# Performance work log

Measured on AMD Instinct MI355X. Metric: run time of the kernel, lower is better.

The kernel has to match this reference:

```python
import jax, jax.numpy as jnp
import numpy as np

BS, NC, C, D, K, ALPHA = 4, 64, 256, 64, 32, 8
H_S, H_M, H_MOD = 256, 256, 256


def setup_inputs() -> dict:
    key = jax.random.key(0)
    ks = jax.random.split(key, 16)
    f = jax.random.normal
    return {
        "h": f(ks[0], (BS, NC, C, D)) * 0.1,
        "prev_messages": f(ks[1], (BS, NC, C, D)) * 0.1,
        "decay_logit": f(ks[2], (BS, NC, C)) * 0.1,
        "primitives_state": f(ks[3], (BS, NC, C, D)) * 0.1,
        "hebbian_traces": f(ks[4], (BS, NC, C, K)) * 0.1,
        "msg_magnitude": f(ks[5], (BS, NC, C)) * 0.1,
        "cc_signals": f(ks[6], (BS, NC * D)),
        "state_w1": f(ks[7], (H_S, 3 * D + 1)) * (2.0 / (3 * D + 1 + H_S)) ** 0.5,
        "state_b1": jnp.zeros((H_S,)),
        "state_w2": f(ks[8], (D, H_S)) * (2.0 / (H_S + D)) ** 0.5,
        "state_b2": jnp.zeros((D,)),
        "msg_w1": f(ks[9], (H_M, 3 * D)) * (2.0 / (3 * D + H_M)) ** 0.5,
        "msg_b1": jnp.zeros((H_M,)),
        "msg_w2": f(ks[10], (D, H_M)) * (2.0 / (H_M + D)) ** 0.5,
        "msg_b2": jnp.zeros((D,)),
        "mod_w1": f(ks[11], (NC, H_MOD, K + 3 * D + 1)) * (2.0 / (K + 3 * D + 1 + H_MOD)) ** 0.5,
        "mod_b1": jnp.zeros((NC, H_MOD)),
        "mod_w2": f(ks[12], (NC, H_MOD, K + 1 + D)) * (2.0 / (H_MOD + K + 1 + D)) ** 0.5,
        "mod_b2": jnp.zeros((NC, K + 1 + D)),
        "neuron_id": f(ks[13], (NC, C, D)) * (1.0 / D ** 0.5),
        "conn_indices": jax.random.randint(ks[14], (NC, C, K), 0, C, dtype=jnp.int32),
    }


def _forward(conn_indices, h, prev_messages, decay_logit, primitives_state,
             hebbian_traces, msg_magnitude, cc_signals,
             state_w1, state_b1, state_w2, state_b2,
             msg_w1, msg_b1, msg_w2, msg_b2,
             mod_w1, mod_b1, mod_w2, mod_b2, neuron_id):
    B = h.shape[0]
    # --- per-cell modulator: aggregate over neurons (dim 2), grouped GEMM over NC cells ---
    h_mean = h.mean(2)                                  # [B,NC,D]
    prim_mean = primitives_state.mean(2)                # [B,NC,D]
    hebb_mean = hebbian_traces.mean(2)                  # [B,NC,K]
    dec_mean = decay_logit.mean(2, keepdims=True)       # [B,NC,1]
    act = jnp.broadcast_to(msg_magnitude.mean(2)[..., None], (B, NC, D))
    mod_in = jnp.concatenate([hebb_mean, h_mean, dec_mean, prim_mean, act], -1)  # [B,NC,K+3D+1]
    hid = jnp.tanh(jnp.einsum('bci,chi->bch', mod_in, mod_w1) + mod_b1)
    out = jnp.einsum('bch,cho->bco', hid, mod_w2) + mod_b2                        # [B,NC,K+1+D]
    w_conn = out[..., :K]          # [B,NC,K] broadcast to all C neurons of the cell
    decay = out[..., K]            # [B,NC]
    prim = out[..., K + 1:]        # [B,NC,D]
    # --- cell-local K-neighbor weighted gather (memory bound) ---
    neigh = prev_messages[:, jnp.arange(NC)[:, None, None], conn_indices]   # [B,NC,C,K,D]
    w_sig = jax.nn.sigmoid(jnp.broadcast_to(w_conn[:, :, None, :], (B, NC, C, K)))
    received = jnp.einsum('bnck,bnckd->bncd', w_sig, neigh)                 # [B,NC,C,D]
    # --- inject external signal into the first ALPHA neurons of each cell ---
    inj = cc_signals.reshape(B, NC, D)[:, :, None, :]
    input_vec = received.at[:, :, :ALPHA, :].add(inj)
    # --- shared state MLP (split-weight formulation as in the original) ---
    prim_b = jnp.broadcast_to(prim[:, :, None, :], input_vec.shape)         # [B,NC,C,D]
    dec_b = jnp.broadcast_to(decay[:, :, None], (B, NC, C))                 # [B,NC,C]
    hid_s = (input_vec @ state_w1[:, :D].T
             + prim_b @ state_w1[:, D:2 * D].T
             + (neuron_id @ state_w1[:, 2 * D:3 * D].T)[None]
             + dec_b[..., None] * state_w1[:, 3 * D]
             + state_b1)
    update = jnp.tanh(jnp.tanh(hid_s) @ state_w2.T + state_b2)              # [B,NC,C,D]
    d = jax.nn.sigmoid(dec_b)[..., None]
    h_new = d * h + (1.0 - d) * update
    # --- shared message MLP ---
    hid_m = jnp.tanh(h_new @ msg_w1[:, :D].T
                     + prim_b @ msg_w1[:, D:2 * D].T
                     + (neuron_id @ msg_w1[:, 2 * D:].T)[None]
                     + msg_b1)
    msg = jnp.tanh(hid_m @ msg_w2.T + msg_b2)                               # [B,NC,C,D]
    # --- readout: last ALPHA neurons per cell, averaged, flattened to D_lm ---
    readout = msg[:, :, C - ALPHA:, :].mean(2).reshape(B, NC * D)
    return readout


def reference(h, prev_messages, decay_logit, primitives_state, hebbian_traces,
              msg_magnitude, cc_signals, state_w1, state_b1, state_w2, state_b2,
              msg_w1, msg_b1, msg_w2, msg_b2, mod_w1, mod_b1, mod_w2, mod_b2,
              neuron_id, conn_indices):
    return _forward(conn_indices, h, prev_messages, decay_logit, primitives_state,
                    hebbian_traces, msg_magnitude, cc_signals,
                    state_w1, state_b1, state_w2, state_b2,
                    msg_w1, msg_b1, msg_w2, msg_b2,
                    mod_w1, mod_b1, mod_w2, mod_b2, neuron_id)
```

## Files before the change

kernel.cpp:

```cpp
#include <hip/hip_runtime.h>
#include <math.h>

#define BS 4
#define NC 64
#define CC 256
#define DD 64
#define KK 32
#define ALPHA 8
#define HS 256
#define HM 256
#define HMOD 256
#define MODIN 225
#define MODOUT 97

__global__ __launch_bounds__(256) void k_means(
    const float* __restrict__ h, const float* __restrict__ dec,
    const float* __restrict__ prim, const float* __restrict__ hebb,
    const float* __restrict__ mmag, float* __restrict__ ws_modin)
{
    const int bn = blockIdx.x >> 2, seg = blockIdx.x & 3;
    const int tid = threadIdx.x;
    __shared__ float4 buf4[256];
    __shared__ float  buf[256];
    const float inv = 1.0f / (float)CC;
    float* mi = ws_modin + (size_t)bn * MODIN;

    if (seg <= 1) {
        const float* src = (seg == 0) ? (h + (size_t)bn * CC * DD)
                                      : (prim + (size_t)bn * CC * DD);
        const int dst = (seg == 0) ? 32 : 97;
        const float4* p4 = (const float4*)src;
        int q = tid & 15, c0 = tid >> 4;
        float4 sum = make_float4(0.f, 0.f, 0.f, 0.f);
        for (int c = c0; c < CC; c += 16) {
            float4 v = p4[c * 16 + q];
            sum.x += v.x; sum.y += v.y; sum.z += v.z; sum.w += v.w;
        }
        buf4[tid] = sum;
        __syncthreads();
        if (tid < 16) {
            float4 t = buf4[tid];
            for (int r = 1; r < 16; r++) {
                float4 v = buf4[r * 16 + tid];
                t.x += v.x; t.y += v.y; t.z += v.z; t.w += v.w;
            }
            mi[dst + tid * 4 + 0] = t.x * inv;
            mi[dst + tid * 4 + 1] = t.y * inv;
            mi[dst + tid * 4 + 2] = t.z * inv;
            mi[dst + tid * 4 + 3] = t.w * inv;
        }
    } else if (seg == 2) {
        const float4* p4 = (const float4*)(hebb + (size_t)bn * CC * KK);
        int q = tid & 7, c0 = tid >> 3;
        float4 sum = make_float4(0.f, 0.f, 0.f, 0.f);
        for (int c = c0; c < CC; c += 32) {
            float4 v = p4[c * 8 + q];
            sum.x += v.x; sum.y += v.y; sum.z += v.z; sum.w += v.w;
        }
        buf4[tid] = sum;
        __syncthreads();
        if (tid < 8) {
            float4 t = buf4[tid];
            for (int r = 1; r < 32; r++) {
                float4 v = buf4[r * 8 + tid];
                t.x += v.x; t.y += v.y; t.z += v.z; t.w += v.w;
            }
            mi[tid * 4 + 0] = t.x * inv;
            mi[tid * 4 + 1] = t.y * inv;
            mi[tid * 4 + 2] = t.z * inv;
            mi[tid * 4 + 3] = t.w * inv;
        }
    } else {
        buf[tid] = dec[(size_t)bn * CC + tid];
        __syncthreads();
        for (int s2 = 128; s2 > 0; s2 >>= 1) {
            if (tid < s2) buf[tid] += buf[tid + s2];
            __syncthreads();
        }
        if (tid == 0) mi[96] = buf[0] * inv;
        __syncthreads();
        buf[tid] = mmag[(size_t)bn * CC + tid];
        __syncthreads();
        for (int s2 = 128; s2 > 0; s2 >>= 1) {
            if (tid < s2) buf[tid] += buf[tid + s2];
            __syncthreads();
        }
        __syncthreads();
        float m = buf[0] * inv;
        if (tid < DD) mi[161 + tid] = m;
    }
}

__global__ __launch_bounds__(256) void k_modhid(
    const float* __restrict__ ws_modin, const float* __restrict__ modw1,
    const float* __restrict__ modb1, float* __restrict__ ws_hid)
{
    const int n = blockIdx.x >> 2, hq = blockIdx.x & 3;
    const int tid = threadIdx.x;
    __shared__ float mi[BS][MODIN];
    for (int i = tid; i < BS * MODIN; i += 256) {
        int b = i / MODIN, j = i - b * MODIN;
        mi[b][j] = ws_modin[(size_t)(b * NC + n) * MODIN + j];
    }
    __syncthreads();
    const int hl = tid >> 2, b = tid & 3;
    const int hh = hq * 64 + hl;
    const float* w = modw1 + ((size_t)n * HMOD + hh) * MODIN;
    float acc = modb1[n * HMOD + hh];
    for (int i = 0; i < MODIN; i++) acc += mi[b][i] * w[i];
    ws_hid[(size_t)(b * NC + n) * HMOD + hh] = tanhf(acc);
}

__global__ __launch_bounds__(256) void k_modout(
    const float* __restrict__ ws_hid, const float* __restrict__ modw2,
    const float* __restrict__ modb2, float* __restrict__ ws_par)
{
    const int n = blockIdx.x, tid = threadIdx.x;
    __shared__ alignas(16) float hid[BS][HMOD];
    for (int i = tid; i < BS * HMOD; i += 256) {
        int b = i >> 8, j = i & 255;
        hid[b][j] = ws_hid[(size_t)(b * NC + n) * HMOD + j];
    }
    __syncthreads();
    const int b = tid & 3, o0 = tid >> 2;
    const int o1 = o0 + 64;
    const bool has1 = (o1 < MODOUT);
    const float* wbase = modw2 + (size_t)n * HMOD * MODOUT;
    float acc0 = modb2[n * MODOUT + o0];
    float acc1 = has1 ? modb2[n * MODOUT + o1] : 0.f;
    const float4* h4 = (const float4*)hid[b];
    for (int t = 0; t < 64; t++) {
        float4 hv = h4[t];
        const float* w = wbase + (size_t)(t * 4) * MODOUT;
        acc0 += hv.x * w[o0] + hv.y * w[MODOUT + o0]
              + hv.z * w[2 * MODOUT + o0] + hv.w * w[3 * MODOUT + o0];
        if (has1)
            acc1 += hv.x * w[o1] + hv.y * w[MODOUT + o1]
                  + hv.z * w[2 * MODOUT + o1] + hv.w * w[3 * MODOUT + o1];
    }
    float* pout = ws_par + (size_t)(b * NC + n) * MODOUT;
    pout[o0] = (o0 < KK) ? (1.0f / (1.0f + expf(-acc0))) : acc0;
    if (has1) pout[o1] = (o1 < KK) ? (1.0f / (1.0f + expf(-acc1))) : acc1;
}

__global__ __launch_bounds__(256) void k_nid(
    const float* __restrict__ nid_g, const float* __restrict__ sw1,
    const float* __restrict__ mw1, float* __restrict__ nts,
    float* __restrict__ ntm)
{
    const int n = blockIdx.x >> 3, a = blockIdx.x & 7;
    const int tid = threadIdx.x;
    __shared__ alignas(16) float nv[DD];
    if (tid < DD) nv[tid] = nid_g[((size_t)n * CC + (CC - ALPHA + a)) * DD + tid];
    __syncthreads();
    const float*  w  = sw1 + (size_t)tid * 193 + 128;
    const float4* wm = (const float4*)(mw1 + (size_t)tid * 192 + 128);
    const float4* n4 = (const float4*)nv;
    float acc = 0.f, accm = 0.f;
    for (int d4 = 0; d4 < 16; d4++) {
        float4 v = n4[d4];
        acc  += v.x * w[d4 * 4] + v.y * w[d4 * 4 + 1]
              + v.z * w[d4 * 4 + 2] + v.w * w[d4 * 4 + 3];
        float4 wv = wm[d4];
        accm += v.x * wv.x + v.y * wv.y + v.z * wv.z + v.w * wv.w;
    }
    nts[((size_t)n * ALPHA + a) * HS + tid] = acc;
    ntm[((size_t)n * ALPHA + a) * HM + tid] = accm;
}

__global__ __launch_bounds__(256) void k_cells(
    const float* __restrict__ h, const float* __restrict__ pm,
    const int* __restrict__ conn,
    const float* __restrict__ sw1, const float* __restrict__ sb1,
    const float* __restrict__ sw2, const float* __restrict__ sb2,
    const float* __restrict__ mw1, const float* __restrict__ mb1,
    const float* __restrict__ mw2, const float* __restrict__ mb2,
    const float* __restrict__ nid_g, const float* __restrict__ ws_par,
    const float* __restrict__ nts, const float* __restrict__ ntm,
    float* __restrict__ out)
{
    const int b = blockIdx.x >> 6, n = blockIdx.x & 63;
    const int tid = threadIdx.x;

    __shared__ float wsig[KK];
    __shared__ alignas(16) float prm[DD];
    __shared__ int cidx[ALPHA][KK];
    __shared__ alignas(16) float nid_s[ALPHA][DD];
    __shared__ alignas(16) float iv[ALPHA][DD];
    __shared__ alignas(16) float hnew[ALPHA][DD];
    __shared__ alignas(16) float t1[ALPHA][HS];
    __shared__ alignas(16) float hm[ALPHA][HM];
    __shared__ float red[256];
    __shared__ float sdecay_sh, ssig_sh;

    const float* par = ws_par + (size_t)(b * NC + n) * MODOUT;
    if (tid < KK) wsig[tid] = par[tid];
    if (tid == KK) {
        float dr = par[KK];
        sdecay_sh = dr;
        ssig_sh = 1.0f / (1.0f + expf(-dr));
    }
    if (tid > KK && tid < MODOUT) prm[tid - KK - 1] = par[tid];
    {
        int a = tid >> 5, k = tid & 31;
        cidx[a][k] = conn[((size_t)n * CC + (CC - ALPHA + a)) * KK + k];
    }
    for (int i = tid; i < ALPHA * DD; i += 256) {
        int a = i >> 6, d = i & 63;
        nid_s[a][d] = nid_g[((size_t)n * CC + (CC - ALPHA + a)) * DD + d];
    }
    __syncthreads();

    float base_s, base_m;
    {
        const float* w  = sw1 + (size_t)tid * 193;
        const float* wm = mw1 + (size_t)tid * 192;
        float acc  = sb1[tid] + sdecay_sh * w[192];
        float accm = mb1[tid];
        for (int d = 0; d < DD; d++) {
            float pv = prm[d];
            acc  += pv * w[64 + d];
            accm += pv * wm[64 + d];
        }
        base_s = acc; base_m = accm;
    }

    const size_t pmbase = (size_t)(b * NC + n) * CC * DD;
    {
        const int d = tid & 63, ag = tid >> 6;
        for (int half = 0; half < 2; half++) {
            int a = ag + half * 4;
            float acc = 0.f;
            for (int k = 0; k < KK; k++)
                acc += wsig[k] * pm[pmbase + (size_t)cidx[a][k] * DD + d];
            iv[a][d] = acc;
        }
    }
    __syncthreads();

    {
        const float* w = sw1 + (size_t)tid * 193;
        float acc[ALPHA];
        if (nts) {
            const float* p = nts + (size_t)n * ALPHA * HS + tid;
            for (int a = 0; a < ALPHA; a++) acc[a] = base_s + p[(size_t)a * HS];
        } else {
            for (int a = 0; a < ALPHA; a++) acc[a] = base_s;
        }
        for (int d4 = 0; d4 < 16; d4++) {
            float w0 = w[d4 * 4], w1 = w[d4 * 4 + 1],
                  w2 = w[d4 * 4 + 2], w3 = w[d4 * 4 + 3];
            for (int a = 0; a < ALPHA; a++) {
                float4 v = ((const float4*)iv[a])[d4];
                acc[a] += v.x * w0 + v.y * w1 + v.z * w2 + v.w * w3;
            }
            if (!nts) {
                float u0 = w[128 + d4 * 4], u1 = w[128 + d4 * 4 + 1],
                      u2 = w[128 + d4 * 4 + 2], u3 = w[128 + d4 * 4 + 3];
                for (int a = 0; a < ALPHA; a++) {
                    float4 v = ((const float4*)nid_s[a])[d4];
                    acc[a] += v.x * u0 + v.y * u1 + v.z * u2 + v.w * u3;
                }
            }
        }
        for (int a = 0; a < ALPHA; a++) t1[a][tid] = tanhf(acc[a]);
    }
    __syncthreads();

    {
        const int d = tid & 63, ag = tid >> 6;
        const float4* w4  = (const float4*)(sw2 + (size_t)d * HS);
        const float4* t40 = (const float4*)t1[ag];
        const float4* t41 = (const float4*)t1[ag + 4];
        float acc0 = 0.f, acc1 = 0.f;
        for (int t = 0; t < 64; t++) {
            float4 wv = w4[t];
            float4 a0 = t40[t], a1 = t41[t];
            acc0 += wv.x * a0.x + wv.y * a0.y + wv.z * a0.z + wv.w * a0.w;
            acc1 += wv.x * a1.x + wv.y * a1.y + wv.z * a1.z + wv.w * a1.w;
        }
        float bb = sb2[d], sg = ssig_sh;
        float u0 = tanhf(acc0 + bb), u1 = tanhf(acc1 + bb);
        float h0 = h[pmbase + (size_t)(CC - ALPHA + ag) * DD + d];
        float h1 = h[pmbase + (size_t)(CC - ALPHA + ag + 4) * DD + d];
        hnew[ag][d]     = sg * h0 + (1.f - sg) * u0;
        hnew[ag + 4][d] = sg * h1 + (1.f - sg) * u1;
    }
    __syncthreads();

    {
        const float4* w4 = (const float4*)(mw1 + (size_t)tid * 192);
        float acc[ALPHA];
        if (ntm) {
            const float* p = ntm + (size_t)n * ALPHA * HM + tid;
            for (int a = 0; a < ALPHA; a++) acc[a] = base_m + p[(size_t)a * HM];
        } else {
            for (int a = 0; a < ALPHA; a++) acc[a] = base_m;
        }
        for (int d4 = 0; d4 < 16; d4++) {
            float4 wv = w4[d4];
            for (int a = 0; a < ALPHA; a++) {
                float4 v = ((const float4*)hnew[a])[d4];
                acc[a] += wv.x * v.x + wv.y * v.y + wv.z * v.z + wv.w * v.w;
            }
            if (!ntm) {
                float4 uv = w4[32 + d4];
                for (int a = 0; a < ALPHA; a++) {
                    float4 v = ((const float4*)nid_s[a])[d4];
                    acc[a] += uv.x * v.x + uv.y * v.y + uv.z * v.z + uv.w * v.w;
                }
            }
        }
        for (int a = 0; a < ALPHA; a++) hm[a][tid] = tanhf(acc[a]);
    }
    __syncthreads();

    {
        const int d = tid & 63, ag = tid >> 6;
        const float4* w4  = (const float4*)(mw2 + (size_t)d * HM);
        const float4* m40 = (const float4*)hm[ag];
        const float4* m41 = (const float4*)hm[ag + 4];
        float acc0 = 0.f, acc1 = 0.f;
        for (int t = 0; t < 64; t++) {
            float4 wv = w4[t];
            float4 a0 = m40[t], a1 = m41[t];
            acc0 += wv.x * a0.x + wv.y * a0.y + wv.z * a0.z + wv.w * a0.w;
            acc1 += wv.x * a1.x + wv.y * a1.y + wv.z * a1.z + wv.w * a1.w;
        }
        float bb = mb2[d];
        red[tid] = tanhf(acc0 + bb) + tanhf(acc1 + bb);
    }
    __syncthreads();
    if (tid < DD)
        out[(size_t)(b * NC + n) * DD + tid] =
            (red[tid] + red[tid + 64] + red[tid + 128] + red[tid + 192]) * 0.125f;
}

extern "C" void kernel_launch(void* const* d_in, const int* in_sizes, int n_in,
                              void* d_out, int out_size, void* d_ws, size_t ws_size,
                              hipStream_t stream) {
    const float* h     = (const float*)d_in[0];
    const float* pm    = (const float*)d_in[1];
    const float* dec   = (const float*)d_in[2];
    const float* prim  = (const float*)d_in[3];
    const float* hebb  = (const float*)d_in[4];
    const float* mmag  = (const float*)d_in[5];
    const float* sw1   = (const float*)d_in[7];
    const float* sb1   = (const float*)d_in[8];
    const float* sw2   = (const float*)d_in[9];
    const float* sb2   = (const float*)d_in[10];
    const float* mw1   = (const float*)d_in[11];
    const float* mb1   = (const float*)d_in[12];
    const float* mw2   = (const float*)d_in[13];
    const float* mb2   = (const float*)d_in[14];
    const float* modw1 = (const float*)d_in[15];
    const float* modb1 = (const float*)d_in[16];
    const float* modw2 = (const float*)d_in[17];
    const float* modb2 = (const float*)d_in[18];
    const float* nid   = (const float*)d_in[19];
    const int*   conn  = (const int*)d_in[20];
    float* out = (float*)d_out;

    float* ws       = (float*)d_ws;
    float* ws_modin = ws;
    float* ws_hid   = ws + 57600;
    float* ws_par   = ws + 57600 + 65536;
    float* nts      = ws + 147968;
    float* ntm      = ws + 147968 + 131072;
    const bool use_nt = ws_size >= (size_t)(147968 + 2 * 131072) * sizeof(float);

    if (use_nt)
        k_nid<<<NC * ALPHA, 256, 0, stream>>>(nid, sw1, mw1, nts, ntm);
    k_means <<<BS * NC * 4, 256, 0, stream>>>(h, dec, prim, hebb, mmag, ws_modin);
    k_modhid<<<NC * 4, 256, 0, stream>>>(ws_modin, modw1, modb1, ws_hid);
    k_modout<<<NC, 256, 0, stream>>>(ws_hid, modw2, modb2, ws_par);
    k_cells <<<BS * NC, 256, 0, stream>>>(h, pm, conn, sw1, sb1, sw2, sb2,
                                          mw1, mb1, mw2, mb2, nid, ws_par,
                                          use_nt ? nts : nullptr,
                                          use_nt ? ntm : nullptr, out);
}
```

Before: 236.3 us.

## Fuse modulator output into cell kernel, widen blocks, split-K modhid per batch

Drops the separate k_modout and k_nid kernels. The modulator output GEMV moves into k_cells, which now runs 1024-thread blocks so the per-stage dot products can be split across more threads and reduced in shared memory. The neuron-id projection is recomputed inline instead of being precomputed. k_modhid now launches one block per batch and hidden quarter, splitting the input dimension four ways to raise parallelism. This trades two fewer launches and more threads per cell for redundant neuron-id and modulator work on each of the BS batch blocks, and for higher register and shared-memory pressure.

```diff
diff --git a/kernel.cpp b/kernel.cpp
--- a/kernel.cpp
+++ b/kernel.cpp
@@ -95,88 +95,39 @@
     const float* __restrict__ ws_modin, const float* __restrict__ modw1,
     const float* __restrict__ modb1, float* __restrict__ ws_hid)
 {
-    const int n = blockIdx.x >> 2, hq = blockIdx.x & 3;
+    const int n = blockIdx.x >> 4, hq = (blockIdx.x >> 2) & 3, b = blockIdx.x & 3;
     const int tid = threadIdx.x;
-    __shared__ float mi[BS][MODIN];
-    for (int i = tid; i < BS * MODIN; i += 256) {
-        int b = i / MODIN, j = i - b * MODIN;
-        mi[b][j] = ws_modin[(size_t)(b * NC + n) * MODIN + j];
-    }
-    __syncthreads();
-    const int hl = tid >> 2, b = tid & 3;
+    __shared__ float mi_s[MODIN + 3];
+    __shared__ float red[64][4];
+    if (tid < MODIN) mi_s[tid] = ws_modin[(size_t)(b * NC + n) * MODIN + tid];
+    __syncthreads();
+
+    const int hl = tid >> 2, kq = tid & 3;
     const int hh = hq * 64 + hl;
     const float* w = modw1 + ((size_t)n * HMOD + hh) * MODIN;
-    float acc = modb1[n * HMOD + hh];
-    for (int i = 0; i < MODIN; i++) acc += mi[b][i] * w[i];
-    ws_hid[(size_t)(b * NC + n) * HMOD + hh] = tanhf(acc);
+    const int i0 = kq * 57, i1 = (kq == 3) ? MODIN : (i0 + 57);
+    float acc = 0.f;
+    #pragma unroll 8
+    for (int i = i0; i < i1; i++) acc += mi_s[i] * w[i];
+    red[hl][kq] = acc;
+    __syncthreads();
+    if (tid < 64) {
+        const int hh2 = hq * 64 + tid;
+        float v = red[tid][0] + red[tid][1] + red[tid][2] + red[tid][3]
+                + modb1[n * HMOD + hh2];
+        ws_hid[(size_t)(b * NC + n) * HMOD + hh2] = tanhf(v);
+    }
 }
 
-__global__ __launch_bounds__(256) void k_modout(
-    const float* __restrict__ ws_hid, const float* __restrict__ modw2,
-    const float* __restrict__ modb2, float* __restrict__ ws_par)
-{
-    const int n = blockIdx.x, tid = threadIdx.x;
-    __shared__ alignas(16) float hid[BS][HMOD];
-    for (int i = tid; i < BS * HMOD; i += 256) {
-        int b = i >> 8, j = i & 255;
-        hid[b][j] = ws_hid[(size_t)(b * NC + n) * HMOD + j];
-    }
-    __syncthreads();
-    const int b = tid & 3, o0 = tid >> 2;
-    const int o1 = o0 + 64;
-    const bool has1 = (o1 < MODOUT);
-    const float* wbase = modw2 + (size_t)n * HMOD * MODOUT;
-    float acc0 = modb2[n * MODOUT + o0];
-    float acc1 = has1 ? modb2[n * MODOUT + o1] : 0.f;
-    const float4* h4 = (const float4*)hid[b];
-    for (int t = 0; t < 64; t++) {
-        float4 hv = h4[t];
-        const float* w = wbase + (size_t)(t * 4) * MODOUT;
-        acc0 += hv.x * w[o0] + hv.y * w[MODOUT + o0]
-              + hv.z * w[2 * MODOUT + o0] + hv.w * w[3 * MODOUT + o0];
-        if (has1)
-            acc1 += hv.x * w[o1] + hv.y * w[MODOUT + o1]
-                  + hv.z * w[2 * MODOUT + o1] + hv.w * w[3 * MODOUT + o1];
-    }
-    float* pout = ws_par + (size_t)(b * NC + n) * MODOUT;
-    pout[o0] = (o0 < KK) ? (1.0f / (1.0f + expf(-acc0))) : acc0;
-    if (has1) pout[o1] = (o1 < KK) ? (1.0f / (1.0f + expf(-acc1))) : acc1;
-}
-
-__global__ __launch_bounds__(256) void k_nid(
-    const float* __restrict__ nid_g, const float* __restrict__ sw1,
-    const float* __restrict__ mw1, float* __restrict__ nts,
-    float* __restrict__ ntm)
-{
-    const int n = blockIdx.x >> 3, a = blockIdx.x & 7;
-    const int tid = threadIdx.x;
-    __shared__ alignas(16) float nv[DD];
-    if (tid < DD) nv[tid] = nid_g[((size_t)n * CC + (CC - ALPHA + a)) * DD + tid];
-    __syncthreads();
-    const float*  w  = sw1 + (size_t)tid * 193 + 128;
-    const float4* wm = (const float4*)(mw1 + (size_t)tid * 192 + 128);
-    const float4* n4 = (const float4*)nv;
-    float acc = 0.f, accm = 0.f;
-    for (int d4 = 0; d4 < 16; d4++) {
-        float4 v = n4[d4];
-        acc  += v.x * w[d4 * 4] + v.y * w[d4 * 4 + 1]
-              + v.z * w[d4 * 4 + 2] + v.w * w[d4 * 4 + 3];
-        float4 wv = wm[d4];
-        accm += v.x * wv.x + v.y * wv.y + v.z * wv.z + v.w * wv.w;
-    }
-    nts[((size_t)n * ALPHA + a) * HS + tid] = acc;
-    ntm[((size_t)n * ALPHA + a) * HM + tid] = accm;
-}
-
-__global__ __launch_bounds__(256) void k_cells(
+__global__ __launch_bounds__(1024) void k_cells(
     const float* __restrict__ h, const float* __restrict__ pm,
     const int* __restrict__ conn,
     const float* __restrict__ sw1, const float* __restrict__ sb1,
     const float* __restrict__ sw2, const float* __restrict__ sb2,
     const float* __restrict__ mw1, const float* __restrict__ mb1,
     const float* __restrict__ mw2, const float* __restrict__ mb2,
-    const float* __restrict__ nid_g, const float* __restrict__ ws_par,
-    const float* __restrict__ nts, const float* __restrict__ ntm,
+    const float* __restrict__ nid_g, const float* __restrict__ ws_hid,
+    const float* __restrict__ modw2, const float* __restrict__ modb2,
     float* __restrict__ out)
 {
     const int b = blockIdx.x >> 6, n = blockIdx.x & 63;
@@ -190,150 +141,173 @@
     __shared__ alignas(16) float hnew[ALPHA][DD];
     __shared__ alignas(16) float t1[ALPHA][HS];
     __shared__ alignas(16) float hm[ALPHA][HM];
-    __shared__ float red[256];
+    __shared__ float red[1024];
+    __shared__ float base_s_sh[HS], base_m_sh[HM];
+    __shared__ float hidv[HMOD];
     __shared__ float sdecay_sh, ssig_sh;
 
-    const float* par = ws_par + (size_t)(b * NC + n) * MODOUT;
-    if (tid < KK) wsig[tid] = par[tid];
-    if (tid == KK) {
-        float dr = par[KK];
-        sdecay_sh = dr;
-        ssig_sh = 1.0f / (1.0f + expf(-dr));
-    }
-    if (tid > KK && tid < MODOUT) prm[tid - KK - 1] = par[tid];
-    {
-        int a = tid >> 5, k = tid & 31;
+    const size_t pmbase = (size_t)(b * NC + n) * CC * DD;
+
+    if (tid < 256) {
+        hidv[tid] = ws_hid[(size_t)(b * NC + n) * HMOD + tid];
+    } else if (tid < 512) {
+        int j = tid - 256, a = j >> 5, k = j & 31;
         cidx[a][k] = conn[((size_t)n * CC + (CC - ALPHA + a)) * KK + k];
-    }
-    for (int i = tid; i < ALPHA * DD; i += 256) {
-        int a = i >> 6, d = i & 63;
+    } else {
+        int j = tid - 512, a = j >> 6, d = j & 63;
         nid_s[a][d] = nid_g[((size_t)n * CC + (CC - ALPHA + a)) * DD + d];
     }
     __syncthreads();
 
-    float base_s, base_m;
-    {
-        const float* w  = sw1 + (size_t)tid * 193;
-        const float* wm = mw1 + (size_t)tid * 192;
-        float acc  = sb1[tid] + sdecay_sh * w[192];
-        float accm = mb1[tid];
-        for (int d = 0; d < DD; d++) {
-            float pv = prm[d];
-            acc  += pv * w[64 + d];
-            accm += pv * wm[64 + d];
-        }
-        base_s = acc; base_m = accm;
-    }
-
-    const size_t pmbase = (size_t)(b * NC + n) * CC * DD;
-    {
-        const int d = tid & 63, ag = tid >> 6;
-        for (int half = 0; half < 2; half++) {
-            int a = ag + half * 4;
-            float acc = 0.f;
-            for (int k = 0; k < KK; k++)
-                acc += wsig[k] * pm[pmbase + (size_t)cidx[a][k] * DD + d];
-            iv[a][d] = acc;
-        }
-    }
-    __syncthreads();
-
-    {
-        const float* w = sw1 + (size_t)tid * 193;
-        float acc[ALPHA];
-        if (nts) {
-            const float* p = nts + (size_t)n * ALPHA * HS + tid;
-            for (int a = 0; a < ALPHA; a++) acc[a] = base_s + p[(size_t)a * HS];
-        } else {
-            for (int a = 0; a < ALPHA; a++) acc[a] = base_s;
-        }
+    {
+        const int o = tid & 127, kq = tid >> 7;
+        float acc = 0.f;
+        if (o < MODOUT) {
+            const float* w = modw2 + ((size_t)n * HMOD + kq * 32) * MODOUT + o;
+            #pragma unroll
+            for (int j = 0; j < 32; j++) acc += hidv[kq * 32 + j] * w[(size_t)j * MODOUT];
+        }
+        red[tid] = acc;
+    }
+    __syncthreads();
+    if (tid < 128) {
+        const int o = tid;
+        if (o < MODOUT) {
+            float v = modb2[n * MODOUT + o];
+            #pragma unroll
+            for (int kq = 0; kq < 8; kq++) v += red[o + 128 * kq];
+            if (o < KK) wsig[o] = 1.0f / (1.0f + expf(-v));
+            else if (o == KK) {
+                sdecay_sh = v;
+                ssig_sh = 1.0f / (1.0f + expf(-v));
+            } else prm[o - KK - 1] = v;
+        }
+    }
+    __syncthreads();
+
+    if (tid < 256) {
+        const int hh = tid;
+        const float* w = sw1 + (size_t)hh * 193;
+        float acc = sb1[hh] + sdecay_sh * w[192];
+        for (int d = 0; d < DD; d++) acc += prm[d] * w[64 + d];
+        base_s_sh[hh] = acc;
+    } else if (tid < 512) {
+        const int hh = tid - 256;
+        const float4* w4 = (const float4*)(mw1 + (size_t)hh * 192 + 64);
+        const float4* p4 = (const float4*)prm;
+        float acc = mb1[hh];
+        #pragma unroll
+        for (int d4 = 0; d4 < 16; d4++) {
+            float4 wv = w4[d4], pv = p4[d4];
+            acc += wv.x * pv.x + wv.y * pv.y + wv.z * pv.z + wv.w * pv.w;
+        }
+        base_m_sh[hh] = acc;
+    } else {
+        const int j = tid - 512, a = j >> 6, d = j & 63;
+        float acc = 0.f;
+        #pragma unroll 8
+        for (int k = 0; k < KK; k++)
+            acc += wsig[k] * pm[pmbase + (size_t)cidx[a][k] * DD + d];
+        iv[a][d] = acc;
+    }
+    __syncthreads();
+
+    {
+        const int hh = tid & 255, g = tid >> 8;
+        const int a0 = g * 2, a1 = g * 2 + 1;
+        const float* w = sw1 + (size_t)hh * 193;
+        float acc0 = base_s_sh[hh], acc1 = acc0;
+        #pragma unroll
         for (int d4 = 0; d4 < 16; d4++) {
             float w0 = w[d4 * 4], w1 = w[d4 * 4 + 1],
                   w2 = w[d4 * 4 + 2], w3 = w[d4 * 4 + 3];
-            for (int a = 0; a < ALPHA; a++) {
-                float4 v = ((const float4*)iv[a])[d4];
-                acc[a] += v.x * w0 + v.y * w1 + v.z * w2 + v.w * w3;
-            }
-            if (!nts) {
-                float u0 = w[128 + d4 * 4], u1 = w[128 + d4 * 4 + 1],
-                      u2 = w[128 + d4 * 4 + 2], u3 = w[128 + d4 * 4 + 3];
-                for (int a = 0; a < ALPHA; a++) {
-                    float4 v = ((const float4*)nid_s[a])[d4];
-                    acc[a] += v.x * u0 + v.y * u1 + v.z * u2 + v.w * u3;
-                }
-            }
-        }
-        for (int a = 0; a < ALPHA; a++) t1[a][tid] = tanhf(acc[a]);
-    }
-    __syncthreads();
-
-    {
-        const int d = tid & 63, ag = tid >> 6;
-        const float4* w4  = (const float4*)(sw2 + (size_t)d * HS);
-        const float4* t40 = (const float4*)t1[ag];
-        const float4* t41 = (const float4*)t1[ag + 4];
-        float acc0 = 0.f, acc1 = 0.f;
-        for (int t = 0; t < 64; t++) {
-            float4 wv = w4[t];
-            float4 a0 = t40[t], a1 = t41[t];
-            acc0 += wv.x * a0.x + wv.y * a0.y + wv.z * a0.z + wv.w * a0.w;
-            acc1 += wv.x * a1.x + wv.y * a1.y + wv.z * a1.z + wv.w * a1.w;
-        }
-        float bb = sb2[d], sg = ssig_sh;
-        float u0 = tanhf(acc0 + bb), u1 = tanhf(acc1 + bb);
-        float h0 = h[pmbase + (size_t)(CC - ALPHA + ag) * DD + d];
-        float h1 = h[pmbase + (size_t)(CC - ALPHA + ag + 4) * DD + d];
-        hnew[ag][d]     = sg * h0 + (1.f - sg) * u0;
-        hnew[ag + 4][d] = sg * h1 + (1.f - sg) * u1;
-    }
-    __syncthreads();
-
-    {
-        const float4* w4 = (const float4*)(mw1 + (size_t)tid * 192);
-        float acc[ALPHA];
-        if (ntm) {
-            const float* p = ntm + (size_t)n * ALPHA * HM + tid;
-            for (int a = 0; a < ALPHA; a++) acc[a] = base_m + p[(size_t)a * HM];
-        } else {
-            for (int a = 0; a < ALPHA; a++) acc[a] = base_m;
-        }
+            float4 v0 = ((const float4*)iv[a0])[d4];
+            float4 v1 = ((const float4*)iv[a1])[d4];
+            acc0 += v0.x * w0 + v0.y * w1 + v0.z * w2 + v0.w * w3;
+            acc1 += v1.x * w0 + v1.y * w1 + v1.z * w2 + v1.w * w3;
+            float u0 = w[128 + d4 * 4], u1 = w[128 + d4 * 4 + 1],
+                  u2 = w[128 + d4 * 4 + 2], u3 = w[128 + d4 * 4 + 3];
+            float4 n0 = ((const float4*)nid_s[a0])[d4];
+            float4 n1 = ((const float4*)nid_s[a1])[d4];
+            acc0 += n0.x * u0 + n0.y * u1 + n0.z * u2 + n0.w * u3;
+            acc1 += n1.x * u0 + n1.y * u1 + n1.z * u2 + n1.w * u3;
+        }
+        t1[a0][hh] = tanhf(acc0);
+        t1[a1][hh] = tanhf(acc1);
+    }
+    __syncthreads();
+
+    {
+        const int d = tid & 63, a = (tid >> 6) & 7, half = tid >> 9;
+        const float4* w4 = (const float4*)(sw2 + (size_t)d * HS + half * 128);
+        const float4* t4 = ((const float4*)t1[a]) + half * 32;
+        float acc = 0.f;
+        #pragma unroll
+        for (int j = 0; j < 32; j++) {
+            float4 wv = w4[j], tv = t4[j];
+            acc += wv.x * tv.x + wv.y * tv.y + wv.z * tv.z + wv.w * tv.w;
+        }
+        red[tid] = acc;
+    }
+    __syncthreads();
+    if (tid < 512) {
+        const int d = tid & 63, a = tid >> 6;
+        float u = tanhf(red[tid] + red[tid + 512] + sb2[d]);
+        float hv = h[pmbase + (size_t)(CC - ALPHA + a) * DD + d];
+        hnew[a][d] = ssig_sh * hv + (1.f - ssig_sh) * u;
+    }
+    __syncthreads();
+
+    {
+        const int hh = tid & 255, g = tid >> 8;
+        const int a0 = g * 2, a1 = g * 2 + 1;
+        const float4* w4 = (const float4*)(mw1 + (size_t)hh * 192);
+        float acc0 = base_m_sh[hh], acc1 = acc0;
+        #pragma unroll
         for (int d4 = 0; d4 < 16; d4++) {
             float4 wv = w4[d4];
-            for (int a = 0; a < ALPHA; a++) {
-                float4 v = ((const float4*)hnew[a])[d4];
-                acc[a] += wv.x * v.x + wv.y * v.y + wv.z * v.z + wv.w * v.w;
-            }
-            if (!ntm) {
-                float4 uv = w4[32 + d4];
-                for (int a = 0; a < ALPHA; a++) {
-                    float4 v = ((const float4*)nid_s[a])[d4];
-                    acc[a] += uv.x * v.x + uv.y * v.y + uv.z * v.z + uv.w * v.w;
-                }
-            }
-        }
-        for (int a = 0; a < ALPHA; a++) hm[a][tid] = tanhf(acc[a]);
-    }
-    __syncthreads();
-
-    {
-        const int d = tid & 63, ag = tid >> 6;
-        const float4* w4  = (const float4*)(mw2 + (size_t)d * HM);
-        const float4* m40 = (const float4*)hm[ag];
-        const float4* m41 = (const float4*)hm[ag + 4];
-        float acc0 = 0.f, acc1 = 0.f;
-        for (int t = 0; t < 64; t++) {
-            float4 wv = w4[t];
-            float4 a0 = m40[t], a1 = m41[t];
-            acc0 += wv.x * a0.x + wv.y * a0.y + wv.z * a0.z + wv.w * a0.w;
-            acc1 += wv.x * a1.x + wv.y * a1.y + wv.z * a1.z + wv.w * a1.w;
-        }
-        float bb = mb2[d];
-        red[tid] = tanhf(acc0 + bb) + tanhf(acc1 + bb);
-    }
-    __syncthreads();
-    if (tid < DD)
-        out[(size_t)(b * NC + n) * DD + tid] =
-            (red[tid] + red[tid + 64] + red[tid + 128] + red[tid + 192]) * 0.125f;
+            float4 v0 = ((const float4*)hnew[a0])[d4];
+            float4 v1 = ((const float4*)hnew[a1])[d4];
+            acc0 += wv.x * v0.x + wv.y * v0.y + wv.z * v0.z + wv.w * v0.w;
+            acc1 += wv.x * v1.x + wv.y * v1.y + wv.z * v1.z + wv.w * v1.w;
+            float4 uv = w4[32 + d4];
+            float4 n0 = ((const float4*)nid_s[a0])[d4];
+            float4 n1 = ((const float4*)nid_s[a1])[d4];
+            acc0 += uv.x * n0.x + uv.y * n0.y + uv.z * n0.z + uv.w * n0.w;
+            acc1 += uv.x * n1.x + uv.y * n1.y + uv.z * n1.z + uv.w * n1.w;
+        }
+        hm[a0][hh] = tanhf(acc0);
+        hm[a1][hh] = tanhf(acc1);
+    }
+    __syncthreads();
+
+    {
+        const int d = tid & 63, a = (tid >> 6) & 7, half = tid >> 9;
+        const float4* w4 = (const float4*)(mw2 + (size_t)d * HM + half * 128);
+        const float4* m4 = ((const float4*)hm[a]) + half * 32;
+        float acc = 0.f;
+        #pragma unroll
+        for (int j = 0; j < 32; j++) {
+            float4 wv = w4[j], mv = m4[j];
+            acc += wv.x * mv.x + wv.y * mv.y + wv.z * mv.z + wv.w * mv.w;
+        }
+        red[tid] = acc;
+    }
+    __syncthreads();
+    float mval = 0.f;
+    if (tid < 512) {
+        const int d = tid & 63;
+        mval = tanhf(red[tid] + red[tid + 512] + mb2[d]);
+    }
+    __syncthreads();
+    if (tid < 512) red[tid] = mval;
+    __syncthreads();
+    if (tid < DD) {
+        float s = 0.f;
+        #pragma unroll
+        for (int a = 0; a < ALPHA; a++) s += red[a * 64 + tid];
+        out[(size_t)(b * NC + n) * DD + tid] = s * 0.125f;
+    }
 }
 
 extern "C" void kernel_launch(void* const* d_in, const int* in_sizes, int n_in,
@@ -364,18 +338,10 @@
     float* ws       = (float*)d_ws;
     float* ws_modin = ws;
     float* ws_hid   = ws + 57600;
-    float* ws_par   = ws + 57600 + 65536;
-    float* nts      = ws + 147968;
-    float* ntm      = ws + 147968 + 131072;
-    const bool use_nt = ws_size >= (size_t)(147968 + 2 * 131072) * sizeof(float);
-
-    if (use_nt)
-        k_nid<<<NC * ALPHA, 256, 0, stream>>>(nid, sw1, mw1, nts, ntm);
+
     k_means <<<BS * NC * 4, 256, 0, stream>>>(h, dec, prim, hebb, mmag, ws_modin);
-    k_modhid<<<NC * 4, 256, 0, stream>>>(ws_modin, modw1, modb1, ws_hid);
-    k_modout<<<NC, 256, 0, stream>>>(ws_hid, modw2, modb2, ws_par);
-    k_cells <<<BS * NC, 256, 0, stream>>>(h, pm, conn, sw1, sb1, sw2, sb2,
-                                          mw1, mb1, mw2, mb2, nid, ws_par,
-                                          use_nt ? nts : nullptr,
-                                          use_nt ? ntm : nullptr, out);
+    k_modhid<<<NC * 4 * BS, 256, 0, stream>>>(ws_modin, modw1, modb1, ws_hid);
+    k_cells <<<BS * NC, 1024, 0, stream>>>(h, pm, conn, sw1, sb1, sw2, sb2,
+                                           mw1, mb1, mw2, mb2, nid, ws_hid,
+                                           modw2, modb2, out);
 }
```

Result: slower. 348.1 us (+47.3%).
